# Performance work log

Hardware: AMD Instinct MI355X
Metric: run time of the kernel (lower is better)

Reference implementation:

```python
import jax, jax.numpy as jnp
import numpy as np

N_BINS = 15


def setup_inputs() -> dict:
    key = jax.random.key(0)
    k1, k2 = jax.random.split(key)
    N, C = 262144, 128
    logits = jax.random.normal(k1, (N, C), dtype=jnp.float32)
    labels = jax.random.randint(k2, (N,), 0, C, dtype=jnp.int64)
    return {"logits": logits, "labels": labels}


def reference(logits, labels):
    # Classwise ECE: for each class i and bin (l, u], accumulate
    # |avg_confidence - accuracy| * prop_in_bin, then mean over classes.
    N, C = logits.shape
    probs = jax.nn.softmax(logits, axis=1)  # [N, C]

    # Bin (k/n_bins, (k+1)/n_bins] -> index k = ceil(p * n_bins) - 1.
    # p == 0 falls in no bin (strict lower bound in torch .gt), mask it out.
    valid = probs > 0.0
    bin_idx = jnp.clip(jnp.ceil(probs * N_BINS).astype(jnp.int32) - 1, 0, N_BINS - 1)

    class_ids = jnp.arange(C, dtype=jnp.int32)[None, :]            # [1, C]
    flat_idx = (class_ids * N_BINS + bin_idx).reshape(-1)           # [N*C]
    num_seg = C * N_BINS

    valid_f = valid.astype(probs.dtype)
    counts = jax.ops.segment_sum(valid_f.reshape(-1), flat_idx, num_segments=num_seg)
    conf_sum = jax.ops.segment_sum((probs * valid_f).reshape(-1), flat_idx, num_segments=num_seg)
    correct = (labels[:, None].astype(jnp.int32) == class_ids).astype(probs.dtype) * valid_f
    acc_sum = jax.ops.segment_sum(correct.reshape(-1), flat_idx, num_segments=num_seg)

    counts = counts.reshape(C, N_BINS)
    conf_sum = conf_sum.reshape(C, N_BINS)
    acc_sum = acc_sum.reshape(C, N_BINS)

    nonempty = counts > 0
    denom = jnp.maximum(counts, 1.0)
    gap = jnp.abs(conf_sum / denom - acc_sum / denom)               # [C, n_bins]
    per_class_sce = jnp.sum(jnp.where(nonempty, gap * counts / N, 0.0), axis=1)  # [C]

    # num_classes = max(labels) + 1; average per-class SCE over that many classes.
    num_classes = jnp.max(labels).astype(jnp.int32) + 1
    class_mask = jnp.arange(C, dtype=jnp.int32) < num_classes
    sce = jnp.sum(jnp.where(class_mask, per_class_sce, 0.0)) / num_classes.astype(probs.dtype)
    return sce
```

## Files before the change

### kernel.cpp

```cpp
#include <hip/hip_runtime.h>
#include <hip/hip_bf16.h>


constexpr int N_BINS  = 15;
constexpr int N_CLS   = 128;
constexpr int BSTRIDE = 16;
constexpr int HCELLS  = N_CLS * BSTRIDE;
constexpr int NSLOT   = 4;
constexpr int BLOCK   = 256;
constexpr int PASSES  = 4;
constexpr int ROWS_PER_BLOCK = 64 * PASSES;
constexpr int WS_WORDS = NSLOT * (3 * HCELLS + N_CLS) + 1;

template <int CTRL>
__device__ __forceinline__ float dpp_f32(float x) {
    return __int_as_float(__builtin_amdgcn_mov_dpp(__float_as_int(x), CTRL, 0xF, 0xF, true));
}
__device__ __forceinline__ float quad_max(float x) {
    x = fmaxf(x, dpp_f32<0xB1>(x));
    x = fmaxf(x, dpp_f32<0x4E>(x));
    return x;
}
__device__ __forceinline__ float quad_sum(float x) {
    x += dpp_f32<0xB1>(x);
    x += dpp_f32<0x4E>(x);
    return x;
}

__global__ void zero_ws_kernel(int* __restrict__ ws, int n) {
    int i = blockIdx.x * blockDim.x + threadIdx.x;
    if (i < n) ws[i] = 0;
}

__global__ __launch_bounds__(BLOCK, 4) void ece_hist_kernel(
        const float* __restrict__ logits, const int* __restrict__ labels,
        int rows, int* __restrict__ ws) {
    __shared__ int   s_cnt[HCELLS];
    __shared__ float s_conf[HCELLS];
    __shared__ int   s_acc[HCELLS];
    __shared__ float s_ptot[N_CLS];
    __shared__ int   s_labmax;

    const int tid  = threadIdx.x;
    const int lane = tid & 63;
    const int q    = tid & 3;
    const int quad = tid >> 2;

    for (int i = tid; i < HCELLS; i += BLOCK) { s_cnt[i] = 0; s_conf[i] = 0.0f; s_acc[i] = 0; }
    for (int i = tid; i < N_CLS; i += BLOCK) s_ptot[i] = 0.0f;
    if (tid == 0) s_labmax = 0;
    __syncthreads();

    float psum[32];
    #pragma unroll
    for (int i = 0; i < 32; ++i) psum[i] = 0.0f;
    int labmax = 0;

    const int rowbase = blockIdx.x * ROWS_PER_BLOCK;

    #pragma unroll 1
    for (int pass = 0; pass < PASSES; ++pass) {
        const int row = rowbase + pass * 64 + quad;
        if (row < rows) {
            float4 f4[8];
            const float4* vp = reinterpret_cast<const float4*>(
                logits + (size_t)row * N_CLS + q * 32);
            #pragma unroll
            for (int k = 0; k < 8; ++k) f4[k] = vp[k];
            float* v = reinterpret_cast<float*>(f4);

            const int lab  = labels[row];
            labmax = max(labmax, lab);
            const int labi = lab & 31;
            const bool qmatch = ((lab >> 5) == q);

            float w[16];
            #pragma unroll
            for (int i = 0; i < 16; ++i) w[i] = fmaxf(v[i], v[i + 16]);
            #pragma unroll
            for (int s = 8; s >= 1; s >>= 1)
                #pragma unroll
                for (int i = 0; i < 8; ++i) if (i < s) w[i] = fmaxf(w[i], w[i + s]);
            const float m = quad_max(w[0]);

            #pragma unroll
            for (int i = 0; i < 32; ++i) v[i] = __expf(v[i] - m);
            float z[16];
            #pragma unroll
            for (int i = 0; i < 16; ++i) z[i] = v[i] + v[i + 16];
            #pragma unroll
            for (int s = 8; s >= 1; s >>= 1)
                #pragma unroll
                for (int i = 0; i < 8; ++i) if (i < s) z[i] = z[i] + z[i + s];
            const float inv = 1.0f / quad_sum(z[0]);

            float p_lab = 0.0f;
            #pragma unroll
            for (int i = 0; i < 32; ++i) {
                const float p = v[i] * inv;
                psum[i] += p;
                const float t15 = p * (float)N_BINS;
                const bool cond = (t15 > 1.0f) || (p == 0.0f);
                p_lab = (i == labi) ? p : p_lab;
                if (__any(cond)) {
                    if (cond) {
                        const int c = q * 32 + i;
                        if (p == 0.0f) {
                            atomicAdd(&s_cnt[c * BSTRIDE + 15], 1);
                        } else {
                            const int b = min((int)ceilf(t15) - 1, N_BINS - 1);
                            atomicAdd(&s_cnt[c * BSTRIDE + b], 1);
                            atomicAdd(&s_conf[c * BSTRIDE + b], p);
                        }
                    }
                }
            }
            if (qmatch && p_lab > 0.0f) {
                const float t15 = p_lab * (float)N_BINS;
                const int b = (t15 <= 1.0f) ? 0 : min((int)ceilf(t15) - 1, N_BINS - 1);
                atomicAdd(&s_acc[(lab & (N_CLS - 1)) * BSTRIDE + b], 1);
            }
        }
    }

    atomicMax(&s_labmax, labmax);

    #pragma unroll
    for (int i = 0; i < 32; ++i) {
        float x = psum[i];
        x += dpp_f32<0x124>(x);
        x += dpp_f32<0x128>(x);
        if ((lane & 12) == 0) atomicAdd(&s_ptot[q * 32 + i], x);
    }
    __syncthreads();

    int* __restrict__ g_cnt  = ws;
    float* __restrict__ g_conf = (float*)(ws + NSLOT * HCELLS);
    int* __restrict__ g_acc  = ws + 2 * NSLOT * HCELLS;
    float* __restrict__ g_ptot = (float*)(ws + 3 * NSLOT * HCELLS);
    int* __restrict__ g_labmax = ws + 3 * NSLOT * HCELLS + NSLOT * N_CLS;
    const int slot = blockIdx.x & (NSLOT - 1);

    for (int i = tid; i < HCELLS; i += BLOCK) {
        const int cv = s_cnt[i];
        if (cv) atomicAdd(&g_cnt[slot * HCELLS + i], cv);
        const float cf = s_conf[i];
        if (cf != 0.0f) unsafeAtomicAdd(&g_conf[slot * HCELLS + i], cf);
        const int av = s_acc[i];
        if (av) atomicAdd(&g_acc[slot * HCELLS + i], av);
    }
    for (int i = tid; i < N_CLS; i += BLOCK) {
        const float pv = s_ptot[i];
        if (pv != 0.0f) unsafeAtomicAdd(&g_ptot[slot * N_CLS + i], pv);
    }
    if (tid == 0) atomicMax(g_labmax, s_labmax);
}

__global__ void ece_final_kernel(const int* __restrict__ ws, float* __restrict__ out, int rows) {
    __shared__ float s_pcs[N_CLS];
    const int c = threadIdx.x;

    const int*   g_cnt  = ws;
    const float* g_conf = (const float*)(ws + NSLOT * HCELLS);
    const int*   g_acc  = ws + 2 * NSLOT * HCELLS;
    const float* g_ptot = (const float*)(ws + 3 * NSLOT * HCELLS);
    const int*   g_labmax = ws + 3 * NSLOT * HCELLS + NSLOT * N_CLS;

    float ptot = 0.0f;
    int   cntb[N_BINS];
    float confb[N_BINS];
    int   accb[N_BINS];
    int   zeros = 0;
    #pragma unroll
    for (int b = 0; b < N_BINS; ++b) { cntb[b] = 0; confb[b] = 0.0f; accb[b] = 0; }

    for (int s = 0; s < NSLOT; ++s) {
        ptot += g_ptot[s * N_CLS + c];
        const int base = s * HCELLS + c * BSTRIDE;
        zeros += g_cnt[base + 15];
        accb[0] += g_acc[base + 0];
        #pragma unroll
        for (int b = 1; b < N_BINS; ++b) {
            cntb[b]  += g_cnt[base + b];
            confb[b] += g_conf[base + b];
            accb[b]  += g_acc[base + b];
        }
    }

    long cnt_rest = 0;
    float conf_rest = 0.0f;
    #pragma unroll
    for (int b = 1; b < N_BINS; ++b) { cnt_rest += cntb[b]; conf_rest += confb[b]; }
    const long cnt0 = (long)rows - cnt_rest - zeros;
    const float conf0 = ptot - conf_rest;

    float pcs = 0.0f;
    if (cnt0 > 0) pcs += fabsf(conf0 - (float)accb[0]);
    #pragma unroll
    for (int b = 1; b < N_BINS; ++b)
        if (cntb[b] > 0) pcs += fabsf(confb[b] - (float)accb[b]);
    s_pcs[c] = pcs / (float)rows;
    __syncthreads();

    if (c == 0) {
        const int nc = *g_labmax + 1;
        float tot = 0.0f;
        for (int j = 0; j < nc && j < N_CLS; ++j) tot += s_pcs[j];
        out[0] = tot / (float)nc;
    }
}

extern "C" void kernel_launch(void* const* d_in, const int* in_sizes, int n_in,
                              void* d_out, int out_size, void* d_ws, size_t ws_size,
                              hipStream_t stream) {
    const float* logits = (const float*)d_in[0];
    const int*   labels = (const int*)d_in[1];
    const int rows = in_sizes[1];

    int* ws = (int*)d_ws;
    hipLaunchKernelGGL(zero_ws_kernel, dim3((WS_WORDS + 255) / 256), dim3(256), 0, stream,
                       ws, WS_WORDS);
    const int grid = (rows + ROWS_PER_BLOCK - 1) / ROWS_PER_BLOCK;
    hipLaunchKernelGGL(ece_hist_kernel, dim3(grid), dim3(BLOCK), 0, stream,
                       logits, labels, rows, ws);
    hipLaunchKernelGGL(ece_final_kernel, dim3(1), dim3(N_CLS), 0, stream,
                       ws, (float*)d_out, rows);
}
```

Measured before the change: 226.7 us.

## Split each row across eight lanes instead of four in histogram kernel

Each row is now processed by 8 threads holding 16 logits each, instead of 4 threads holding 32, with the softmax max and sum reductions extended to an 8-lane DPP pattern. Blocks now cover 256 rows in 8 passes of 32 rows, and the launch-bounds occupancy hint is removed. Per-thread partial probability sums go straight to shared atomics without the earlier cross-quad DPP pre-reduction. The aim is lower register pressure and more parallelism per row. The cost is more reduction steps and twice as many shared atomics for the per-class totals.

```diff
diff --git a/kernel.cpp b/kernel.cpp
--- a/kernel.cpp
+++ b/kernel.cpp
@@ -8,22 +8,25 @@
 constexpr int HCELLS  = N_CLS * BSTRIDE;
 constexpr int NSLOT   = 4;
 constexpr int BLOCK   = 256;
-constexpr int PASSES  = 4;
-constexpr int ROWS_PER_BLOCK = 64 * PASSES;
+constexpr int ROWS_PER_PASS  = BLOCK / 8;
+constexpr int PASSES  = 8;
+constexpr int ROWS_PER_BLOCK = ROWS_PER_PASS * PASSES;
 constexpr int WS_WORDS = NSLOT * (3 * HCELLS + N_CLS) + 1;
 
 template <int CTRL>
 __device__ __forceinline__ float dpp_f32(float x) {
     return __int_as_float(__builtin_amdgcn_mov_dpp(__float_as_int(x), CTRL, 0xF, 0xF, true));
 }
-__device__ __forceinline__ float quad_max(float x) {
+__device__ __forceinline__ float dpp8_max(float x) {
     x = fmaxf(x, dpp_f32<0xB1>(x));
     x = fmaxf(x, dpp_f32<0x4E>(x));
+    x = fmaxf(x, dpp_f32<0x141>(x));
     return x;
 }
-__device__ __forceinline__ float quad_sum(float x) {
+__device__ __forceinline__ float dpp8_sum(float x) {
     x += dpp_f32<0xB1>(x);
     x += dpp_f32<0x4E>(x);
+    x += dpp_f32<0x141>(x);
     return x;
 }
 
@@ -32,7 +35,7 @@
     if (i < n) ws[i] = 0;
 }
 
-__global__ __launch_bounds__(BLOCK, 4) void ece_hist_kernel(
+__global__ __launch_bounds__(BLOCK) void ece_hist_kernel(
         const float* __restrict__ logits, const int* __restrict__ labels,
         int rows, int* __restrict__ ws) {
     __shared__ int   s_cnt[HCELLS];
@@ -41,62 +44,61 @@
     __shared__ float s_ptot[N_CLS];
     __shared__ int   s_labmax;
 
-    const int tid  = threadIdx.x;
-    const int lane = tid & 63;
-    const int q    = tid & 3;
-    const int quad = tid >> 2;
+    const int tid = threadIdx.x;
+    const int o   = tid & 7;
+    const int r   = tid >> 3;
 
     for (int i = tid; i < HCELLS; i += BLOCK) { s_cnt[i] = 0; s_conf[i] = 0.0f; s_acc[i] = 0; }
     for (int i = tid; i < N_CLS; i += BLOCK) s_ptot[i] = 0.0f;
     if (tid == 0) s_labmax = 0;
     __syncthreads();
 
-    float psum[32];
-    #pragma unroll
-    for (int i = 0; i < 32; ++i) psum[i] = 0.0f;
+    float psum[16];
+    #pragma unroll
+    for (int i = 0; i < 16; ++i) psum[i] = 0.0f;
     int labmax = 0;
 
     const int rowbase = blockIdx.x * ROWS_PER_BLOCK;
 
     #pragma unroll 1
     for (int pass = 0; pass < PASSES; ++pass) {
-        const int row = rowbase + pass * 64 + quad;
+        const int row = rowbase + pass * ROWS_PER_PASS + r;
         if (row < rows) {
-            float4 f4[8];
             const float4* vp = reinterpret_cast<const float4*>(
-                logits + (size_t)row * N_CLS + q * 32);
-            #pragma unroll
-            for (int k = 0; k < 8; ++k) f4[k] = vp[k];
-            float* v = reinterpret_cast<float*>(f4);
-
-            const int lab  = labels[row];
+                logits + (size_t)row * N_CLS + o * 16);
+            const float4 a = vp[0], b = vp[1], c4 = vp[2], d = vp[3];
+            float v[16];
+            v[0]=a.x;  v[1]=a.y;  v[2]=a.z;  v[3]=a.w;
+            v[4]=b.x;  v[5]=b.y;  v[6]=b.z;  v[7]=b.w;
+            v[8]=c4.x; v[9]=c4.y; v[10]=c4.z; v[11]=c4.w;
+            v[12]=d.x; v[13]=d.y; v[14]=d.z; v[15]=d.w;
+
+            const int lab = labels[row];
             labmax = max(labmax, lab);
-            const int labi = lab & 31;
-            const bool qmatch = ((lab >> 5) == q);
-
-            float w[16];
-            #pragma unroll
-            for (int i = 0; i < 16; ++i) w[i] = fmaxf(v[i], v[i + 16]);
-            #pragma unroll
-            for (int s = 8; s >= 1; s >>= 1)
-                #pragma unroll
-                for (int i = 0; i < 8; ++i) if (i < s) w[i] = fmaxf(w[i], w[i + s]);
-            const float m = quad_max(w[0]);
-
-            #pragma unroll
-            for (int i = 0; i < 32; ++i) v[i] = __expf(v[i] - m);
-            float z[16];
-            #pragma unroll
-            for (int i = 0; i < 16; ++i) z[i] = v[i] + v[i + 16];
-            #pragma unroll
-            for (int s = 8; s >= 1; s >>= 1)
-                #pragma unroll
-                for (int i = 0; i < 8; ++i) if (i < s) z[i] = z[i] + z[i + s];
-            const float inv = 1.0f / quad_sum(z[0]);
+            const int labo = lab >> 4;
+            const int labi = lab & 15;
+
+            float m8[8];
+            #pragma unroll
+            for (int i = 0; i < 8; ++i) m8[i] = fmaxf(v[i], v[i + 8]);
+            float m4a = fmaxf(m8[0], m8[4]), m4b = fmaxf(m8[1], m8[5]);
+            float m4c = fmaxf(m8[2], m8[6]), m4d = fmaxf(m8[3], m8[7]);
+            float m = fmaxf(fmaxf(m4a, m4b), fmaxf(m4c, m4d));
+            m = dpp8_max(m);
+
+            #pragma unroll
+            for (int i = 0; i < 16; ++i) v[i] = __expf(v[i] - m);
+            float z8[8];
+            #pragma unroll
+            for (int i = 0; i < 8; ++i) z8[i] = v[i] + v[i + 8];
+            float z4a = z8[0] + z8[4], z4b = z8[1] + z8[5];
+            float z4c = z8[2] + z8[6], z4d = z8[3] + z8[7];
+            float s = (z4a + z4b) + (z4c + z4d);
+            const float inv = 1.0f / dpp8_sum(s);
 
             float p_lab = 0.0f;
             #pragma unroll
-            for (int i = 0; i < 32; ++i) {
+            for (int i = 0; i < 16; ++i) {
                 const float p = v[i] * inv;
                 psum[i] += p;
                 const float t15 = p * (float)N_BINS;
@@ -104,7 +106,7 @@
                 p_lab = (i == labi) ? p : p_lab;
                 if (__any(cond)) {
                     if (cond) {
-                        const int c = q * 32 + i;
+                        const int c = o * 16 + i;
                         if (p == 0.0f) {
                             atomicAdd(&s_cnt[c * BSTRIDE + 15], 1);
                         } else {
@@ -115,30 +117,24 @@
                     }
                 }
             }
-            if (qmatch && p_lab > 0.0f) {
+            if (o == labo && p_lab > 0.0f) {
                 const float t15 = p_lab * (float)N_BINS;
                 const int b = (t15 <= 1.0f) ? 0 : min((int)ceilf(t15) - 1, N_BINS - 1);
-                atomicAdd(&s_acc[(lab & (N_CLS - 1)) * BSTRIDE + b], 1);
+                atomicAdd(&s_acc[lab * BSTRIDE + b], 1);
             }
         }
     }
 
     atomicMax(&s_labmax, labmax);
-
-    #pragma unroll
-    for (int i = 0; i < 32; ++i) {
-        float x = psum[i];
-        x += dpp_f32<0x124>(x);
-        x += dpp_f32<0x128>(x);
-        if ((lane & 12) == 0) atomicAdd(&s_ptot[q * 32 + i], x);
-    }
+    #pragma unroll
+    for (int i = 0; i < 16; ++i) atomicAdd(&s_ptot[o * 16 + i], psum[i]);
     __syncthreads();
 
-    int* __restrict__ g_cnt  = ws;
-    float* __restrict__ g_conf = (float*)(ws + NSLOT * HCELLS);
-    int* __restrict__ g_acc  = ws + 2 * NSLOT * HCELLS;
-    float* __restrict__ g_ptot = (float*)(ws + 3 * NSLOT * HCELLS);
-    int* __restrict__ g_labmax = ws + 3 * NSLOT * HCELLS + NSLOT * N_CLS;
+    int*   __restrict__ g_cnt    = ws;
+    float* __restrict__ g_conf   = (float*)(ws + NSLOT * HCELLS);
+    int*   __restrict__ g_acc    = ws + 2 * NSLOT * HCELLS;
+    float* __restrict__ g_ptot   = (float*)(ws + 3 * NSLOT * HCELLS);
+    int*   __restrict__ g_labmax = ws + 3 * NSLOT * HCELLS + NSLOT * N_CLS;
     const int slot = blockIdx.x & (NSLOT - 1);
 
     for (int i = tid; i < HCELLS; i += BLOCK) {
@@ -160,10 +156,10 @@
     __shared__ float s_pcs[N_CLS];
     const int c = threadIdx.x;
 
-    const int*   g_cnt  = ws;
-    const float* g_conf = (const float*)(ws + NSLOT * HCELLS);
-    const int*   g_acc  = ws + 2 * NSLOT * HCELLS;
-    const float* g_ptot = (const float*)(ws + 3 * NSLOT * HCELLS);
+    const int*   g_cnt    = ws;
+    const float* g_conf   = (const float*)(ws + NSLOT * HCELLS);
+    const int*   g_acc    = ws + 2 * NSLOT * HCELLS;
+    const float* g_ptot   = (const float*)(ws + 3 * NSLOT * HCELLS);
     const int*   g_labmax = ws + 3 * NSLOT * HCELLS + NSLOT * N_CLS;
 
     float ptot = 0.0f;
@@ -187,11 +183,11 @@
         }
     }
 
-    long cnt_rest = 0;
+    long  cnt_rest = 0;
     float conf_rest = 0.0f;
     #pragma unroll
     for (int b = 1; b < N_BINS; ++b) { cnt_rest += cntb[b]; conf_rest += confb[b]; }
-    const long cnt0 = (long)rows - cnt_rest - zeros;
+    const long  cnt0  = (long)rows - cnt_rest - zeros;
     const float conf0 = ptot - conf_rest;
 
     float pcs = 0.0f;
```

Measured after the change: 224.2 us. About the same (-1.1%).
